# Performance work log

Measured on AMD Instinct MI355X. Metric: run time of the kernel, lower is better.

## Reference

```python
import jax, jax.numpy as jnp
import numpy as np

B, S, HID, NH, HD, INTER, NB = 4, 4096, 2048, 32, 64, 8192, 8
EPS = 1e-5
MEM_EPS = 1e-6


def rmsnorm(x, w, eps=EPS):
    return x * jax.lax.rsqrt(jnp.mean(x * x, axis=-1, keepdims=True) + eps) * w


def hbit_linear(x, w):
    # BitNet b1.58: ternary weights (absmean scale) + int8 per-token activation quant (STE).
    ws = jnp.mean(jnp.abs(w)) + 1e-8
    wq = jnp.round(jnp.clip(w / ws, -1.0, 1.0)) * ws
    w_eff = w + jax.lax.stop_gradient(wq - w)
    xs = 127.0 / jnp.clip(jnp.max(jnp.abs(x), axis=-1, keepdims=True), 1e-5, None)
    xq = jnp.clip(jnp.round(x * xs), -128.0, 127.0) / xs
    x_eff = x + jax.lax.stop_gradient(xq - x)
    return x_eff @ w_eff.T


def infini_attention(xn, wq, wk, wv, wo, beta):
    # xn: [B,S,HID]; segment-wise causal local attention + compressive linear memory.
    def proj(w):
        return (xn @ w.T).reshape(B, S, NH, HD).transpose(0, 2, 1, 3)  # [B,H,S,D]

    q, k, v = proj(wq), proj(wk), proj(wv)
    seg = S // NB

    def to_segs(t):
        return t.reshape(B, NH, NB, seg, HD).transpose(2, 0, 1, 3, 4)  # [NB,B,H,seg,D]

    qs, ks, vs = to_segs(q), to_segs(k), to_segs(v)
    mask = jnp.tril(jnp.ones((seg, seg), bool))
    g = jax.nn.sigmoid(beta)[None, :, None, None]  # per-head memory/local mix
    scale = 1.0 / np.sqrt(HD)

    def step(carry, inp):
        M, z = carry  # M:[B,H,D,D], z:[B,H,D]
        qc, kc, vc = inp
        sq = jax.nn.elu(qc) + 1.0
        sk = jax.nn.elu(kc) + 1.0
        a_mem = jnp.einsum('bhsd,bhde->bhse', sq, M) / (
            jnp.einsum('bhsd,bhd->bhs', sq, z)[..., None] + MEM_EPS)
        scores = jnp.einsum('bhqd,bhkd->bhqk', qc, kc) * scale
        scores = jnp.where(mask, scores, -1e9)
        a_loc = jnp.einsum('bhqk,bhkd->bhqd', jax.nn.softmax(scores, axis=-1), vc)
        M = M + jnp.einsum('bhsd,bhse->bhde', sk, vc)
        z = z + sk.sum(axis=2)
        out = g * a_mem + (1.0 - g) * a_loc
        return (M, z), out

    M0 = jnp.zeros((B, NH, HD, HD), xn.dtype)
    z0 = jnp.zeros((B, NH, HD), xn.dtype)
    _, outs = jax.lax.scan(step, (M0, z0), (qs, ks, vs))  # [NB,B,H,seg,D]
    out = outs.transpose(1, 2, 0, 3, 4).reshape(B, NH, S, HD)
    out = out.transpose(0, 2, 1, 3).reshape(B, S, HID)
    return out @ wo.T


def setup_inputs() -> dict:
    key = jax.random.key(0)
    ks = jax.random.split(key, 12)
    std = 0.02
    return {
        'x': jax.random.normal(ks[0], (B, S, HID), jnp.float32),
        'wq': jax.random.normal(ks[1], (HID, HID), jnp.float32) * std,
        'wk': jax.random.normal(ks[2], (HID, HID), jnp.float32) * std,
        'wv': jax.random.normal(ks[3], (HID, HID), jnp.float32) * std,
        'wo': jax.random.normal(ks[4], (HID, HID), jnp.float32) * std,
        'beta': jnp.zeros((NH,), jnp.float32),
        'gate': jnp.zeros((1,), jnp.float32),
        'attn_norm_w': jnp.ones((HID,), jnp.float32),
        'mlp_norm_w': jnp.ones((HID,), jnp.float32),
        'attn_res_norm_w': jnp.ones((HID,), jnp.float32),
        'attn_res_scale': jnp.full((1,), 0.1, jnp.float32),
        'mlp_res_norm_w': jnp.ones((HID,), jnp.float32),
        'mlp_res_scale': jnp.full((1,), 0.1, jnp.float32),
        'ffn_up_w': jax.random.normal(ks[5], (2 * INTER, HID), jnp.float32) * std,
        'ffn_down_w': jax.random.normal(ks[6], (HID, INTER), jnp.float32) * std,
    }


def reference(x, wq, wk, wv, wo, beta, gate, attn_norm_w, mlp_norm_w,
              attn_res_norm_w, attn_res_scale, mlp_res_norm_w, mlp_res_scale,
              ffn_up_w, ffn_down_w):
    residual = x
    xn = rmsnorm(x, attn_norm_w)
    infini_out = infini_attention(xn, wq, wk, wv, wo, beta)
    gated = jax.nn.sigmoid(gate) * infini_out
    x = residual + attn_res_scale * rmsnorm(gated, attn_res_norm_w)
    residual = x
    xn = rmsnorm(x, mlp_norm_w)
    up = hbit_linear(xn, ffn_up_w)
    gate_up, value = jnp.split(up, 2, axis=-1)
    mlp_out = hbit_linear(jax.nn.silu(gate_up) * value, ffn_down_w)
    x = residual + mlp_res_scale * rmsnorm(mlp_out, mlp_res_norm_w)
    return x
```

## Files before the change

### kernel.cpp

```cpp
#include <hip/hip_runtime.h>
#include <cstdint>
#include <cstddef>

typedef unsigned int u32;
typedef unsigned short u16;
typedef __bf16 bf16x8 __attribute__((ext_vector_type(8)));
typedef float f32x4 __attribute__((ext_vector_type(4)));
typedef float f32x16 __attribute__((ext_vector_type(16)));
typedef int i32x4 __attribute__((ext_vector_type(4)));

#define DEV static __device__ __forceinline__

DEV float bf2f(u16 u) { u32 x = ((u32)u) << 16; return __builtin_bit_cast(float, x); }
DEV u16 f2bf(float f) {
  u32 u = __builtin_bit_cast(u32, f);
  u32 r = (u + 0x7fffu + ((u >> 16) & 1u)) >> 16;
  return (u16)r;
}
DEV u32 pkbf(float a, float b) {
  __bf16 ba = (__bf16)a, bb = (__bf16)b;
  return (u32)__builtin_bit_cast(u16, ba) | ((u32)__builtin_bit_cast(u16, bb) << 16);
}
DEV u32 pk4i8(float a, float b, float c, float d) {
  return (u32)(unsigned char)(char)a | ((u32)(unsigned char)(char)b << 8) |
         ((u32)(unsigned char)(char)c << 16) | ((u32)(unsigned char)(char)d << 24);
}
DEV void bf8tof(const uint4 v, float* f) {
  f[0] = bf2f((u16)(v.x & 0xffffu)); f[1] = bf2f((u16)(v.x >> 16));
  f[2] = bf2f((u16)(v.y & 0xffffu)); f[3] = bf2f((u16)(v.y >> 16));
  f[4] = bf2f((u16)(v.z & 0xffffu)); f[5] = bf2f((u16)(v.z >> 16));
  f[6] = bf2f((u16)(v.w & 0xffffu)); f[7] = bf2f((u16)(v.w >> 16));
}
DEV uint4 f8tobf(const float* f) {
  uint4 r;
  r.x = (u32)f2bf(f[0]) | ((u32)f2bf(f[1]) << 16);
  r.y = (u32)f2bf(f[2]) | ((u32)f2bf(f[3]) << 16);
  r.z = (u32)f2bf(f[4]) | ((u32)f2bf(f[5]) << 16);
  r.w = (u32)f2bf(f[6]) | ((u32)f2bf(f[7]) << 16);
  return r;
}
DEV float sigmoidf_(float x) { return 1.f / (1.f + expf(-x)); }

DEV float wred_sum(float v) {
  #pragma unroll
  for (int m = 32; m; m >>= 1) v += __shfl_xor(v, m, 64);
  return v;
}
DEV float wred_max(float v) {
  #pragma unroll
  for (int m = 32; m; m >>= 1) v = fmaxf(v, __shfl_xor(v, m, 64));
  return v;
}
DEV float block_sum(float v, float* red, int nw) {
  v = wred_sum(v);
  int w = threadIdx.x >> 6, l = threadIdx.x & 63;
  if (l == 0) red[w] = v;
  __syncthreads();
  float t = red[0];
  for (int i = 1; i < nw; ++i) t += red[i];
  __syncthreads();
  return t;
}
DEV float block_max(float v, float* red, int nw) {
  v = wred_max(v);
  int w = threadIdx.x >> 6, l = threadIdx.x & 63;
  if (l == 0) red[w] = v;
  __syncthreads();
  float t = red[0];
  for (int i = 1; i < nw; ++i) t = fmaxf(t, red[i]);
  __syncthreads();
  return t;
}
DEV void gload16(const void* g, void* l) {
  __builtin_amdgcn_global_load_lds((const __attribute__((address_space(1))) void*)g,
                                   (__attribute__((address_space(3))) void*)l, 16, 0, 0);
}
DEV bf16x8 ldfrag(const u16* p) {
  uint4 u = *(const uint4*)p;
  return __builtin_bit_cast(bf16x8, u);
}

#define BN_ 4
#define S_ 4096
#define HID_ 2048
#define NH_ 32
#define HD_ 64
#define INTER_ 8192
#define NBSEG_ 8
#define SEG_ 512
#define TOK_ 16384
#define CHROWS_ 4096

__global__ __launch_bounds__(256) void castf2b(const float* __restrict__ a, u16* __restrict__ o) {
  size_t idx = ((size_t)blockIdx.x * 256 + threadIdx.x) * 4;
  float4 v = *(const float4*)(a + idx);
  float f[4] = {v.x, v.y, v.z, v.w};
  uint2 r;
  r.x = (u32)f2bf(f[0]) | ((u32)f2bf(f[1]) << 16);
  r.y = (u32)f2bf(f[2]) | ((u32)f2bf(f[3]) << 16);
  *(uint2*)(o + idx) = r;
}

__global__ __launch_bounds__(256) void absmean_part(const float* __restrict__ w, float* __restrict__ part) {
  __shared__ float red[4];
  size_t base = (size_t)blockIdx.x * 16384 + threadIdx.x * 4;
  float s = 0.f;
  #pragma unroll
  for (int i = 0; i < 16; ++i) {
    float4 v = *(const float4*)(w + base + (size_t)i * 1024);
    s += fabsf(v.x) + fabsf(v.y) + fabsf(v.z) + fabsf(v.w);
  }
  float t = block_sum(s, red, 4);
  if (threadIdx.x == 0) part[blockIdx.x] = t;
}

__global__ __launch_bounds__(256) void absmean_fin(const float* __restrict__ part, int n, float invN, float* __restrict__ outp) {
  __shared__ float red[4];
  float s = 0.f;
  for (int i = threadIdx.x; i < n; i += 256) s += part[i];
  float t = block_sum(s, red, 4);
  if (threadIdx.x == 0) outp[0] = t * invN + 1e-8f;
}

__global__ __launch_bounds__(256) void ternarize_i8(const float* __restrict__ w, const float* __restrict__ wsp, char* __restrict__ o) {
  size_t idx = ((size_t)blockIdx.x * 256 + threadIdx.x) * 4;
  const float inv = 1.f / wsp[0];
  float4 v = *(const float4*)(w + idx);
  float q0 = rintf(fminf(fmaxf(v.x * inv, -1.f), 1.f));
  float q1 = rintf(fminf(fmaxf(v.y * inv, -1.f), 1.f));
  float q2 = rintf(fminf(fmaxf(v.z * inv, -1.f), 1.f));
  float q3 = rintf(fminf(fmaxf(v.w * inv, -1.f), 1.f));
  *(u32*)(o + idx) = pk4i8(q0, q1, q2, q3);
}

__global__ __launch_bounds__(256) void rmsnorm_cast(const float* __restrict__ x, const float* __restrict__ wn, u16* __restrict__ o) {
  __shared__ float red[4];
  const int r = blockIdx.x, tid = threadIdx.x;
  const float* xr = x + (size_t)r * HID_;
  float vx[8];
  #pragma unroll
  for (int i = 0; i < 2; ++i) {
    float4 t = *(const float4*)(xr + tid * 8 + i * 4);
    vx[i * 4 + 0] = t.x; vx[i * 4 + 1] = t.y; vx[i * 4 + 2] = t.z; vx[i * 4 + 3] = t.w;
  }
  float ss = 0.f;
  #pragma unroll
  for (int j = 0; j < 8; ++j) ss += vx[j] * vx[j];
  float tot = block_sum(ss, red, 4);
  float rstd = rsqrtf(tot * (1.f / HID_) + 1e-5f);
  float wv[8];
  #pragma unroll
  for (int i = 0; i < 2; ++i) {
    float4 t = *(const float4*)(wn + tid * 8 + i * 4);
    wv[i * 4 + 0] = t.x; wv[i * 4 + 1] = t.y; wv[i * 4 + 2] = t.z; wv[i * 4 + 3] = t.w;
  }
  float ov[8];
  #pragma unroll
  for (int j = 0; j < 8; ++j) ov[j] = vx[j] * rstd * wv[j];
  *(uint4*)(o + (size_t)r * HID_ + tid * 8) = f8tobf(ov);
}

__global__ __launch_bounds__(256) void resid1_rms2(const float* __restrict__ x, const u16* __restrict__ ao,
    const float* __restrict__ gatep, const float* __restrict__ w1, const float* __restrict__ rsp,
    const float* __restrict__ w2, float* __restrict__ x2, char* __restrict__ xq, float* __restrict__ xs1) {
  __shared__ float red[4];
  const int r = blockIdx.x, tid = threadIdx.x;
  const float g = sigmoidf_(gatep[0]);
  const float rs = rsp[0];
  uint4 av = *(const uint4*)(ao + (size_t)r * HID_ + tid * 8);
  float f[8]; bf8tof(av, f);
  float ss = 0.f;
  #pragma unroll
  for (int j = 0; j < 8; ++j) { f[j] *= g; ss += f[j] * f[j]; }
  float tot = block_sum(ss, red, 4);
  float rstd1 = rsqrtf(tot * (1.f / HID_) + 1e-5f);
  const float* xr = x + (size_t)r * HID_;
  float xv2[8];
  #pragma unroll
  for (int i = 0; i < 2; ++i) {
    float4 xv = *(const float4*)(xr + tid * 8 + i * 4);
    float4 wv = *(const float4*)(w1 + tid * 8 + i * 4);
    xv2[i * 4 + 0] = xv.x + rs * f[i * 4 + 0] * rstd1 * wv.x;
    xv2[i * 4 + 1] = xv.y + rs * f[i * 4 + 1] * rstd1 * wv.y;
    xv2[i * 4 + 2] = xv.z + rs * f[i * 4 + 2] * rstd1 * wv.z;
    xv2[i * 4 + 3] = xv.w + rs * f[i * 4 + 3] * rstd1 * wv.w;
  }
  float* o = x2 + (size_t)r * HID_;
  *(float4*)(o + tid * 8) = float4{xv2[0], xv2[1], xv2[2], xv2[3]};
  *(float4*)(o + tid * 8 + 4) = float4{xv2[4], xv2[5], xv2[6], xv2[7]};
  float ss2 = 0.f;
  #pragma unroll
  for (int j = 0; j < 8; ++j) ss2 += xv2[j] * xv2[j];
  float tot2 = block_sum(ss2, red, 4);
  float rstd2 = rsqrtf(tot2 * (1.f / HID_) + 1e-5f);
  float xn[8]; float mx = 0.f;
  #pragma unroll
  for (int i = 0; i < 2; ++i) {
    float4 wv = *(const float4*)(w2 + tid * 8 + i * 4);
    xn[i * 4 + 0] = xv2[i * 4 + 0] * rstd2 * wv.x;
    xn[i * 4 + 1] = xv2[i * 4 + 1] * rstd2 * wv.y;
    xn[i * 4 + 2] = xv2[i * 4 + 2] * rstd2 * wv.z;
    xn[i * 4 + 3] = xv2[i * 4 + 3] * rstd2 * wv.w;
  }
  #pragma unroll
  for (int j = 0; j < 8; ++j) mx = fmaxf(mx, fabsf(xn[j]));
  float bm = block_max(mx, red, 4);
  float xs = 127.f / fmaxf(bm, 1e-5f);
  float q[8];
  #pragma unroll
  for (int j = 0; j < 8; ++j) q[j] = fminf(fmaxf(rintf(xn[j] * xs), -128.f), 127.f);
  uint2 pw;
  pw.x = pk4i8(q[0], q[1], q[2], q[3]);
  pw.y = pk4i8(q[4], q[5], q[6], q[7]);
  *(uint2*)(xq + (size_t)r * HID_ + tid * 8) = pw;
  if (tid == 0) xs1[r] = xs;
}

__global__ __launch_bounds__(256) void quant_h_i8(const u16* __restrict__ hb, char* __restrict__ hq, float* __restrict__ xs2) {
  __shared__ float red[4];
  const int r = blockIdx.x, tid = threadIdx.x;
  const u16* hr = hb + (size_t)r * INTER_ + tid * 32;
  float f[32];
  #pragma unroll
  for (int k = 0; k < 4; ++k) {
    uint4 v = *(const uint4*)(hr + k * 8);
    bf8tof(v, &f[k * 8]);
  }
  float mx = 0.f;
  #pragma unroll
  for (int j = 0; j < 32; ++j) mx = fmaxf(mx, fabsf(f[j]));
  float bm = block_max(mx, red, 4);
  float xs = 127.f / fmaxf(bm, 1e-5f);
  u32 pw[8];
  #pragma unroll
  for (int k = 0; k < 8; ++k) {
    float q[4];
    #pragma unroll
    for (int j = 0; j < 4; ++j) q[j] = fminf(fmaxf(rintf(f[k * 4 + j] * xs), -128.f), 127.f);
    pw[k] = pk4i8(q[0], q[1], q[2], q[3]);
  }
  char* oq = hq + (size_t)r * INTER_ + tid * 32;
  *(uint4*)oq = uint4{pw[0], pw[1], pw[2], pw[3]};
  *(uint4*)(oq + 16) = uint4{pw[4], pw[5], pw[6], pw[7]};
  if (tid == 0) xs2[r] = xs;
}

__global__ __launch_bounds__(256) void final_resid(const float* __restrict__ x2, const u16* __restrict__ mlp,
    const float* __restrict__ wn, const float* __restrict__ rsp, float* __restrict__ out) {
  __shared__ float red[4];
  const int r = blockIdx.x, tid = threadIdx.x;
  const float rs = rsp[0];
  uint4 mv = *(const uint4*)(mlp + (size_t)r * HID_ + tid * 8);
  float f[8]; bf8tof(mv, f);
  float ss = 0.f;
  #pragma unroll
  for (int j = 0; j < 8; ++j) ss += f[j] * f[j];
  float tot = block_sum(ss, red, 4);
  float rstd = rsqrtf(tot * (1.f / HID_) + 1e-5f);
  const float* xr = x2 + (size_t)r * HID_;
  float* o = out + (size_t)r * HID_;
  #pragma unroll
  for (int i = 0; i < 2; ++i) {
    float4 xv = *(const float4*)(xr + tid * 8 + i * 4);
    float4 wv = *(const float4*)(wn + tid * 8 + i * 4);
    float4 ov;
    ov.x = xv.x + rs * f[i * 4 + 0] * rstd * wv.x;
    ov.y = xv.y + rs * f[i * 4 + 1] * rstd * wv.y;
    ov.z = xv.z + rs * f[i * 4 + 2] * rstd * wv.z;
    ov.w = xv.w + rs * f[i * 4 + 3] * rstd * wv.w;
    *(float4*)(o + tid * 8 + i * 4) = ov;
  }
}

template<int MODE>
__global__ __launch_bounds__(256)
void gemm_bt(const u16* __restrict__ A, const u16* __restrict__ Bw, u16* __restrict__ C,
             int N, int K, const float* __restrict__ wsp, const float* __restrict__ xs) {
  __shared__ __align__(16) u16 As[128 * 32];
  __shared__ __align__(16) u16 Bs[128 * 32];
  const int tid = threadIdx.x;
  const int wv = tid >> 6, lane = tid & 63;
  const int l15 = lane & 15, l4 = lane >> 4;
  const int wr = (wv >> 1) * 64, wc = (wv & 1) * 64;
  const int bm = blockIdx.x, bn = blockIdx.y;
  const u16* Ag = A + (size_t)bm * 128 * K;
  const u16* Bg = Bw + (size_t)bn * 128 * K;
  const int c0 = tid, c1 = tid + 256;
  f32x4 acc[4][4] = {};
  for (int kk = 0; kk < K; kk += 32) {
    gload16(Ag + (size_t)(c0 >> 2) * K + kk + (c0 & 3) * 8, &As[c0 * 8]);
    gload16(Ag + (size_t)(c1 >> 2) * K + kk + (c1 & 3) * 8, &As[c1 * 8]);
    gload16(Bg + (size_t)(c0 >> 2) * K + kk + (c0 & 3) * 8, &Bs[c0 * 8]);
    gload16(Bg + (size_t)(c1 >> 2) * K + kk + (c1 & 3) * 8, &Bs[c1 * 8]);
    __syncthreads();
    bf16x8 af[4], bb[4];
    #pragma unroll
    for (int i = 0; i < 4; ++i) af[i] = ldfrag(&As[(wr + i * 16 + l15) * 32 + l4 * 8]);
    #pragma unroll
    for (int j = 0; j < 4; ++j) bb[j] = ldfrag(&Bs[(wc + j * 16 + l15) * 32 + l4 * 8]);
    #pragma unroll
    for (int i = 0; i < 4; ++i)
      #pragma unroll
      for (int j = 0; j < 4; ++j)
        acc[i][j] = __builtin_amdgcn_mfma_f32_16x16x32_bf16(af[i], bb[j], acc[i][j], 0, 0, 0);
    __syncthreads();
  }
  #pragma unroll
  for (int i = 0; i < 4; ++i) {
    #pragma unroll
    for (int r = 0; r < 4; ++r) {
      const int row = bm * 128 + wr + i * 16 + l4 * 4 + r;
      #pragma unroll
      for (int j = 0; j < 4; ++j) {
        const int col = bn * 128 + wc + j * 16 + l15;
        C[(size_t)row * N + col] = f2bf(acc[i][j][r]);
      }
    }
  }
}

__global__ __launch_bounds__(512, 2)
void gemm_up_i8(const char* __restrict__ A, const char* __restrict__ Bw, u16* __restrict__ H,
                const float* __restrict__ wsp, const float* __restrict__ xs) {
  const int K = HID_;
  __shared__ __align__(16) char As[128 * 128];
  __shared__ __align__(16) char Gs[128 * 128];
  __shared__ __align__(16) char Vs[128 * 128];
  const int tid = threadIdx.x;
  const int w = tid >> 6, lane = tid & 63;
  const int l15 = lane & 15, l4 = lane >> 4;
  const int wr = (w >> 2) * 64, wc = (w & 3) * 32;
  int id = blockIdx.x;
  const int cpx = (int)gridDim.x >> 3;
  id = (id & 7) * cpx + (id >> 3);
  const int bm = id & 31, bn = id >> 5;
  const char* Ag = A + (size_t)bm * 128 * K;
  const char* Gg = Bw + (size_t)bn * 128 * K;
  const char* Vg = Bw + ((size_t)INTER_ + bn * 128) * K;
  i32x4 ag[4][2] = {}, av[4][2] = {};
  for (int kk = 0; kk < K; kk += 128) {
    #pragma unroll
    for (int p = 0; p < 2; ++p) {
      const int idx = tid + p * 512;
      const int row = idx >> 3, slot = idx & 7;
      const int ss = slot ^ (row & 7);
      gload16(Ag + (size_t)row * K + kk + ss * 16, &As[idx * 16]);
      gload16(Gg + (size_t)row * K + kk + ss * 16, &Gs[idx * 16]);
      gload16(Vg + (size_t)row * K + kk + ss * 16, &Vs[idx * 16]);
    }
    __syncthreads();
    i32x4 af_[4][2], gf_[2][2], vf_[2][2];
    #pragma unroll
    for (int i = 0; i < 4; ++i) {
      const int r = wr + i * 16 + l15;
      #pragma unroll
      for (int k2 = 0; k2 < 2; ++k2) {
        const int j = k2 * 4 + l4;
        af_[i][k2] = *(const i32x4*)&As[r * 128 + ((j ^ (r & 7)) * 16)];
      }
    }
    #pragma unroll
    for (int jj = 0; jj < 2; ++jj) {
      const int r = wc + jj * 16 + l15;
      #pragma unroll
      for (int k2 = 0; k2 < 2; ++k2) {
        const int j = k2 * 4 + l4;
        gf_[jj][k2] = *(const i32x4*)&Gs[r * 128 + ((j ^ (r & 7)) * 16)];
        vf_[jj][k2] = *(const i32x4*)&Vs[r * 128 + ((j ^ (r & 7)) * 16)];
      }
    }
    #pragma unroll
    for (int i = 0; i < 4; ++i)
      #pragma unroll
      for (int jj = 0; jj < 2; ++jj)
        #pragma unroll
        for (int k2 = 0; k2 < 2; ++k2) {
          ag[i][jj] = __builtin_amdgcn_mfma_i32_16x16x64_i8(af_[i][k2], gf_[jj][k2], ag[i][jj], 0, 0, 0);
          av[i][jj] = __builtin_amdgcn_mfma_i32_16x16x64_i8(af_[i][k2], vf_[jj][k2], av[i][jj], 0, 0, 0);
        }
    __syncthreads();
  }
  const float ws0 = wsp[0];
  #pragma unroll
  for (int i = 0; i < 4; ++i) {
    #pragma unroll
    for (int r = 0; r < 4; ++r) {
      const int row = bm * 128 + wr + i * 16 + l4 * 4 + r;
      const float scl = ws0 / xs[row];
      #pragma unroll
      for (int jj = 0; jj < 2; ++jj) {
        const int col = bn * 128 + wc + jj * 16 + l15;
        const float og = (float)ag[i][jj][r] * scl;
        const float ov = (float)av[i][jj][r] * scl;
        const float hv = og * ov / (1.f + expf(-og));
        H[(size_t)row * INTER_ + col] = f2bf(hv);
      }
    }
  }
}

__global__ __launch_bounds__(256, 2)
void gemm_dn_i8(const char* __restrict__ A, const char* __restrict__ Bw, u16* __restrict__ C,
                const float* __restrict__ wsp, const float* __restrict__ xs) {
  const int N = HID_, K = INTER_;
  __shared__ __align__(16) char As[128 * 128];
  __shared__ __align__(16) char Bs[128 * 128];
  const int tid = threadIdx.x;
  const int wv = tid >> 6, lane = tid & 63;
  const int l15 = lane & 15, l4 = lane >> 4;
  const int wr = (wv >> 1) * 64, wc = (wv & 1) * 64;
  const int bm = blockIdx.x, bn = blockIdx.y;
  const char* Ag = A + (size_t)bm * 128 * K;
  const char* Bg = Bw + (size_t)bn * 128 * K;
  i32x4 acc[4][4] = {};
  for (int kk = 0; kk < K; kk += 128) {
    #pragma unroll
    for (int p = 0; p < 4; ++p) {
      const int idx = tid + p * 256;
      const int row = idx >> 3, slot = idx & 7;
      const int ss = slot ^ (row & 7);
      gload16(Ag + (size_t)row * K + kk + ss * 16, &As[idx * 16]);
      gload16(Bg + (size_t)row * K + kk + ss * 16, &Bs[idx * 16]);
    }
    __syncthreads();
    i32x4 af_[4][2], bb_[4][2];
    #pragma unroll
    for (int i = 0; i < 4; ++i) {
      const int ra = wr + i * 16 + l15;
      const int rb = wc + i * 16 + l15;
      #pragma unroll
      for (int k2 = 0; k2 < 2; ++k2) {
        const int j = k2 * 4 + l4;
        af_[i][k2] = *(const i32x4*)&As[ra * 128 + ((j ^ (ra & 7)) * 16)];
        bb_[i][k2] = *(const i32x4*)&Bs[rb * 128 + ((j ^ (rb & 7)) * 16)];
      }
    }
    #pragma unroll
    for (int i = 0; i < 4; ++i)
      #pragma unroll
      for (int j = 0; j < 4; ++j)
        #pragma unroll
        for (int k2 = 0; k2 < 2; ++k2)
          acc[i][j] = __builtin_amdgcn_mfma_i32_16x16x64_i8(af_[i][k2], bb_[j][k2], acc[i][j], 0, 0, 0);
    __syncthreads();
  }
  const float ws0 = wsp[0];
  #pragma unroll
  for (int i = 0; i < 4; ++i) {
    #pragma unroll
    for (int r = 0; r < 4; ++r) {
      const int row = bm * 128 + wr + i * 16 + l4 * 4 + r;
      const float scl = ws0 / xs[row];
      #pragma unroll
      for (int j = 0; j < 4; ++j) {
        const int col = bn * 128 + wc + j * 16 + l15;
        C[(size_t)row * N + col] = f2bf((float)acc[i][j][r] * scl);
      }
    }
  }
}

DEV void write_otile(const f32x16 oc, float invl, char* stgB, u16* alocrow,
                     int da, int l31, int hi, int lane) {
  #pragma unroll
  for (int r = 0; r < 16; ++r) {
    const int dl = (r & 3) + 8 * (r >> 2) + 4 * hi;
    *(u16*)(stgB + l31 * 64 + ((dl * 2) ^ ((l31 & 3) << 4))) = f2bf(oc[r] * invl);
  }
  #pragma unroll
  for (int p = 0; p < 2; ++p) {
    const int s = lane >> 1;
    const int d8 = (lane & 1) * 8 + p * 16;
    const uint4 val = *(const uint4*)(stgB + s * 64 + ((d8 * 2) ^ ((s & 3) << 4)));
    *(uint4*)(alocrow + (size_t)s * HD_ + da * 32 + d8) = val;
  }
}

__global__ __launch_bounds__(512)
void attn_local_mfma(const u16* __restrict__ q, const u16* __restrict__ k, const u16* __restrict__ v,
                     u16* __restrict__ aloc, float* __restrict__ Useg, float* __restrict__ yseg) {
  __shared__ __align__(16) u16 Ks[512 * 64];
  __shared__ __align__(16) u16 VT[64 * 512];
  __shared__ __align__(16) u16 SP[9216];
  const int bid = blockIdx.x;
  const int c = bid >> 7, bh = bid & 127;
  const int b = bh >> 5, h = bh & 31;
  const int tid = threadIdx.x, w = tid >> 6, lane = tid & 63;
  const int l31 = lane & 31, hi = lane >> 5;
  const size_t rowbase = ((size_t)b * S_ + c * SEG_) * (size_t)HID_ + h * HD_;
  const u16* qg = q + rowbase;
  const u16* kg = k + rowbase;
  const u16* vg = v + rowbase;
  char* KsB = (char*)Ks;
  char* VTB = (char*)VT;
  #pragma unroll
  for (int p = 0; p < 8; ++p) {
    const int idx = tid + p * 512;
    const int t = idx >> 3, dg = idx & 7;
    const uint4 kv = *(const uint4*)(kg + (size_t)t * HID_ + dg * 8);
    *(uint4*)(KsB + t * 128 + ((dg * 16) ^ ((t & 7) << 4))) = kv;
  }
  {
    const int t = w * 64 + lane;
    #pragma unroll
    for (int dg = 0; dg < 8; ++dg) {
      const uint4 vv = *(const uint4*)(vg + (size_t)t * HID_ + dg * 8);
      const u16* e = (const u16*)&vv;
      #pragma unroll
      for (int j = 0; j < 8; ++j) {
        const int d = dg * 8 + j;
        *(u16*)(VTB + d * 1024 + ((t * 2) ^ ((d & 7) << 4))) = e[j];
      }
    }
  }
  uint4 qf[2][4];
  #pragma unroll
  for (int qi = 0; qi < 2; ++qi)
    #pragma unroll
    for (int ks = 0; ks < 4; ++ks)
      qf[qi][ks] = *(const uint4*)(qg + (size_t)(w * 64 + qi * 32 + l31) * HID_ + ks * 16 + hi * 8);
  __syncthreads();

  const size_t arow = (size_t)(b * NH_ + h) * S_ + c * SEG_;
  const int swzk = (l31 & 7) << 4;
  char* stgB = (char*)SP + w * 2048;
  #pragma unroll
  for (int qi = 0; qi < 2; ++qi) {
    f32x16 o0 = {}, o1 = {};
    float m = -3e38f, l = 0.f;
    const int nb = w * 2 + qi + 1;
    for (int tb = 0; tb < nb; ++tb) {
      f32x16 st = {};
      #pragma unroll
      for (int ks = 0; ks < 4; ++ks) {
        const uint4 ka = *(const uint4*)(KsB + (tb * 32 + l31) * 128 + (((ks * 16 + hi * 8) * 2) ^ swzk));
        st = __builtin_amdgcn_mfma_f32_32x32x16_bf16(__builtin_bit_cast(bf16x8, ka),
                                                     __builtin_bit_cast(bf16x8, qf[qi][ks]), st, 0, 0, 0);
      }
      if (tb == nb - 1) {
        #pragma unroll
        for (int r = 0; r < 16; ++r) {
          const int tl = (r & 3) + 8 * (r >> 2) + 4 * hi;
          if (tl > l31) st[r] = -3e38f;
        }
      }
      float tm = st[0];
      #pragma unroll
      for (int r = 1; r < 16; ++r) tm = fmaxf(tm, st[r]);
      tm = fmaxf(tm, __shfl_xor(tm, 32, 64));
      const float mn = fmaxf(m, tm);
      const float fac = __expf((m - mn) * 0.125f);
      float pr[16]; float ps = 0.f;
      #pragma unroll
      for (int r = 0; r < 16; ++r) { pr[r] = __expf((st[r] - mn) * 0.125f); ps += pr[r]; }
      ps += __shfl_xor(ps, 32, 64);
      l = l * fac + ps;
      m = mn;
      #pragma unroll
      for (int r = 0; r < 16; ++r) { o0[r] *= fac; o1[r] *= fac; }
      #pragma unroll
      for (int c2 = 0; c2 < 2; ++c2) {
        const int bi = c2 * 8;
        const u32 a0 = pkbf(pr[bi + 0], pr[bi + 1]);
        const u32 a1 = pkbf(pr[bi + 2], pr[bi + 3]);
        const u32 a2 = pkbf(pr[bi + 4], pr[bi + 5]);
        const u32 a3 = pkbf(pr[bi + 6], pr[bi + 7]);
        const u32 x0 = (u32)__shfl_xor((int)a0, 32, 64);
        const u32 x1 = (u32)__shfl_xor((int)a1, 32, 64);
        const u32 x2 = (u32)__shfl_xor((int)a2, 32, 64);
        const u32 x3 = (u32)__shfl_xor((int)a3, 32, 64);
        uint4 pw;
        pw.x = hi ? x2 : a0;
        pw.y = hi ? x3 : a1;
        pw.z = hi ? a2 : x0;
        pw.w = hi ? a3 : x1;
        const bf16x8 pfr = __builtin_bit_cast(bf16x8, pw);
        const int tO = (tb * 32 + c2 * 16 + hi * 8) * 2;
        const uint4 v0 = *(const uint4*)(VTB + l31 * 1024 + (tO ^ swzk));
        const uint4 v1 = *(const uint4*)(VTB + (32 + l31) * 1024 + (tO ^ swzk));
        o0 = __builtin_amdgcn_mfma_f32_32x32x16_bf16(__builtin_bit_cast(bf16x8, v0), pfr, o0, 0, 0, 0);
        o1 = __builtin_amdgcn_mfma_f32_32x32x16_bf16(__builtin_bit_cast(bf16x8, v1), pfr, o1, 0, 0, 0);
      }
    }
    const float invl = 1.f / l;
    u16* alocrow = aloc + (arow + w * 64 + qi * 32) * HD_;
    write_otile(o0, invl, stgB, alocrow, 0, l31, hi, lane);
    write_otile(o1, invl, stgB, alocrow, 1, l31, hi, lane);
  }

  __syncthreads();
  float* Ured = (float*)SP;
  float* yred = (float*)((char*)SP + 16384);
  for (int i = tid; i < 4096; i += 512) Ured[i] = 0.f;
  yred[tid] = 0.f;
  __syncthreads();
  f32x16 u00 = {}, u01 = {}, u10 = {}, u11 = {};
  float y0 = 0.f, y1 = 0.f;
  #pragma unroll
  for (int kc = 0; kc < 4; ++kc) {
    const int t0 = w * 64 + kc * 16 + hi * 8;
    uint4 af[2];
    #pragma unroll
    for (int da2 = 0; da2 < 2; ++da2) {
      const int d = da2 * 32 + l31;
      u32 wds[4];
      #pragma unroll
      for (int jp = 0; jp < 4; ++jp) {
        const int ta = t0 + jp * 2;
        const int tb2 = ta + 1;
        const float kfa = bf2f(*(const u16*)(KsB + ta * 128 + ((d * 2) ^ ((ta & 7) << 4))));
        const float kfb = bf2f(*(const u16*)(KsB + tb2 * 128 + ((d * 2) ^ ((tb2 & 7) << 4))));
        const float sa = kfa > 0.f ? kfa + 1.f : __expf(kfa);
        const float sb = kfb > 0.f ? kfb + 1.f : __expf(kfb);
        if (da2 == 0) y0 += sa + sb; else y1 += sa + sb;
        wds[jp] = pkbf(sa, sb);
      }
      af[da2].x = wds[0]; af[da2].y = wds[1]; af[da2].z = wds[2]; af[da2].w = wds[3];
    }
    const int tO = t0 * 2;
    const uint4 vb0 = *(const uint4*)(VTB + l31 * 1024 + (tO ^ swzk));
    const uint4 vb1 = *(const uint4*)(VTB + (32 + l31) * 1024 + (tO ^ swzk));
    const bf16x8 a0f = __builtin_bit_cast(bf16x8, af[0]);
    const bf16x8 a1f = __builtin_bit_cast(bf16x8, af[1]);
    const bf16x8 b0f = __builtin_bit_cast(bf16x8, vb0);
    const bf16x8 b1f = __builtin_bit_cast(bf16x8, vb1);
    u00 = __builtin_amdgcn_mfma_f32_32x32x16_bf16(a0f, b0f, u00, 0, 0, 0);
    u01 = __builtin_amdgcn_mfma_f32_32x32x16_bf16(a0f, b1f, u01, 0, 0, 0);
    u10 = __builtin_amdgcn_mfma_f32_32x32x16_bf16(a1f, b0f, u10, 0, 0, 0);
    u11 = __builtin_amdgcn_mfma_f32_32x32x16_bf16(a1f, b1f, u11, 0, 0, 0);
  }
  y0 += __shfl_xor(y0, 32, 64);
  y1 += __shfl_xor(y1, 32, 64);
  if (hi == 0) { yred[w * 64 + l31] = y0; yred[w * 64 + 32 + l31] = y1; }
  for (int ww = 0; ww < 8; ++ww) {
    if (w == ww) {
      #pragma unroll
      for (int r = 0; r < 16; ++r) {
        const int dl = (r & 3) + 8 * (r >> 2) + 4 * hi;
        Ured[dl * 64 + l31]            += u00[r];
        Ured[dl * 64 + 32 + l31]       += u01[r];
        Ured[(32 + dl) * 64 + l31]     += u10[r];
        Ured[(32 + dl) * 64 + 32 + l31]+= u11[r];
      }
    }
    __syncthreads();
  }
  float* Ug = Useg + (size_t)(c * 128 + bh) * 4096;
  for (int i = tid; i < 4096; i += 512) Ug[i] = Ured[i];
  if (tid < 64) {
    float a2 = 0.f;
    #pragma unroll
    for (int ww = 0; ww < 8; ++ww) a2 += yred[ww * 64 + tid];
    yseg[(size_t)(c * 128 + bh) * 64 + tid] = a2;
  }
}

__global__ __launch_bounds__(256)
void attn_prefix(const float* __restrict__ Useg, const float* __restrict__ yseg,
                 float* __restrict__ Mpre, float* __restrict__ zpre) {
  const int bh = blockIdx.x, tid = threadIdx.x;
  for (int idx = tid; idx < 4096; idx += 256) {
    float a2 = 0.f;
    #pragma unroll
    for (int c = 0; c < 8; ++c) {
      const size_t o = ((size_t)(c * 128 + bh)) * 4096 + idx;
      Mpre[o] = a2;
      a2 += Useg[o];
    }
  }
  if (tid < 64) {
    float a2 = 0.f;
    #pragma unroll
    for (int c = 0; c < 8; ++c) {
      const size_t o = ((size_t)(c * 128 + bh)) * 64 + tid;
      zpre[o] = a2;
      a2 += yseg[o];
    }
  }
}

__global__ __launch_bounds__(512)
void attn_combine(const u16* __restrict__ q, const u16* __restrict__ aloc,
                  const float* __restrict__ Mpre, const float* __restrict__ zpre,
                  const float* __restrict__ beta, u16* __restrict__ attno) {
  __shared__ __align__(16) u16 MbT[64 * 64];
  __shared__ float z_lds[64];
  __shared__ float amem[8][16 * 65];
  const int bid = blockIdx.x;
  const int c = bid >> 7, bh = bid & 127;
  const int b = bh >> 5, h = bh & 31;
  const int tid = threadIdx.x, w = tid >> 6, lane = tid & 63;
  const int l15 = lane & 15, l4 = lane >> 4;
  const size_t pre = (size_t)(c * 128 + bh);
  char* MbB = (char*)MbT;
  for (int i = tid; i < 4096; i += 512) {
    const int d = i >> 6, e = i & 63;
    *(u16*)(MbB + (((e * 64 + d) * 2) ^ ((e & 7) << 4))) = f2bf(Mpre[pre * 4096 + i]);
  }
  if (tid < 64) z_lds[tid] = zpre[pre * 64 + tid];
  __syncthreads();
  bf16x8 bb[2][4];
  #pragma unroll
  for (int ks = 0; ks < 2; ++ks)
    #pragma unroll
    for (int jt = 0; jt < 4; ++jt) {
      const int e = jt * 16 + l15;
      const uint4 u = *(const uint4*)(MbB + (((e * 64 + ks * 32 + l4 * 8) * 2) ^ ((e & 7) << 4)));
      bb[ks][jt] = __builtin_bit_cast(bf16x8, u);
    }
  const float g = sigmoidf_(beta[h]);
  const float og = 1.f - g;
  const u16* qg = q + ((size_t)b * S_ + c * SEG_) * HID_ + h * HD_;
  const size_t arow = (size_t)(b * NH_ + h) * S_ + c * SEG_;
  u16* orow = attno + ((size_t)b * S_ + c * SEG_) * HID_ + h * HD_;
  const int rr = lane >> 2, cq = (lane & 3) * 16;
  #pragma unroll
  for (int mi = 0; mi < 4; ++mi) {
    const int s0 = w * 64 + mi * 16;
    f32x4 acc[4] = {};
    float pd = 0.f;
    #pragma unroll
    for (int ks = 0; ks < 2; ++ks) {
      const uint4 qv = *(const uint4*)(qg + (size_t)(s0 + l15) * HID_ + ks * 32 + l4 * 8);
      float f[8]; bf8tof(qv, f);
      float sq[8];
      #pragma unroll
      for (int j = 0; j < 8; ++j) {
        sq[j] = f[j] > 0.f ? f[j] + 1.f : __expf(f[j]);
        pd = fmaf(sq[j], z_lds[ks * 32 + l4 * 8 + j], pd);
      }
      uint4 pw;
      pw.x = pkbf(sq[0], sq[1]); pw.y = pkbf(sq[2], sq[3]);
      pw.z = pkbf(sq[4], sq[5]); pw.w = pkbf(sq[6], sq[7]);
      const bf16x8 af = __builtin_bit_cast(bf16x8, pw);
      #pragma unroll
      for (int jt = 0; jt < 4; ++jt)
        acc[jt] = __builtin_amdgcn_mfma_f32_16x16x32_bf16(af, bb[ks][jt], acc[jt], 0, 0, 0);
    }
    pd += __shfl_xor(pd, 16, 64);
    pd += __shfl_xor(pd, 32, 64);
    pd += 1e-6f;
    float dinv[4];
    #pragma unroll
    for (int r = 0; r < 4; ++r) dinv[r] = 1.f / __shfl(pd, l4 * 4 + r, 64);
    #pragma unroll
    for (int jt = 0; jt < 4; ++jt)
      #pragma unroll
      for (int r = 0; r < 4; ++r)
        amem[w][(l4 * 4 + r) * 65 + jt * 16 + l15] = acc[jt][r] * dinv[r];
    const int s = s0 + rr;
    const u16* alr = aloc + (arow + s) * HD_ + cq;
    const uint4 a0 = *(const uint4*)alr;
    const uint4 a1 = *(const uint4*)(alr + 8);
    float alf[16];
    bf8tof(a0, alf); bf8tof(a1, alf + 8);
    float ov[16];
    #pragma unroll
    for (int t = 0; t < 16; ++t)
      ov[t] = g * amem[w][rr * 65 + cq + t] + og * alf[t];
    *(uint4*)(orow + (size_t)s * HID_ + cq) = f8tobf(ov);
    *(uint4*)(orow + (size_t)s * HID_ + cq + 8) = f8tobf(ov + 8);
  }
}

extern "C" void kernel_launch(void* const* d_in, const int* in_sizes, int n_in,
                              void* d_out, int out_size, void* d_ws, size_t ws_size,
                              hipStream_t stream) {
  const float* x    = (const float*)d_in[0];
  const float* wq   = (const float*)d_in[1];
  const float* wk   = (const float*)d_in[2];
  const float* wv   = (const float*)d_in[3];
  const float* wo   = (const float*)d_in[4];
  const float* beta = (const float*)d_in[5];
  const float* gate = (const float*)d_in[6];
  const float* anw  = (const float*)d_in[7];
  const float* mnw  = (const float*)d_in[8];
  const float* arnw = (const float*)d_in[9];
  const float* arsc = (const float*)d_in[10];
  const float* mrnw = (const float*)d_in[11];
  const float* mrsc = (const float*)d_in[12];
  const float* fup  = (const float*)d_in[13];
  const float* fdn  = (const float*)d_in[14];

  char* W = (char*)d_ws;
  const size_t MB = 1ull << 20;
  u16*   xn1   = (u16*)(W + 0);
  u16*   attno = (u16*)(W + 0);
  u16*   mlpb  = (u16*)(W + 0);
  u16*   qb    = (u16*)(W + 64 * MB);
  char*  xq1   = (char*)(W + 64 * MB);
  u16*   kb    = (u16*)(W + 128 * MB);
  u16*   aob   = (u16*)(W + 128 * MB);
  u16*   hbuf  = (u16*)(W + 128 * MB);
  u16*   vb    = (u16*)(W + 192 * MB);
  u16*   alocb = (u16*)(W + 256 * MB);
  float* x2    = (float*)(W + 192 * MB);
  float* Useg  = (float*)(W + 320 * MB);
  float* Mpre  = (float*)(W + 336 * MB);
  float* yseg  = (float*)(W + 352 * MB);
  float* zpre  = (float*)(W + 352 * MB + 262144);
  float* xs1   = (float*)(W + 352 * MB + 524288);
  float* xs2   = (float*)(W + 352 * MB + 589824);
  float* wsu   = (float*)(W + 352 * MB + 655360);
  float* wsd   = (float*)(W + 352 * MB + 655616);
  float* partU = (float*)(W + 352 * MB + 655872);
  float* partD = (float*)(W + 352 * MB + 664064);
  u16*   w16q  = (u16*)(W + 353 * MB);
  u16*   w16k  = (u16*)(W + 361 * MB);
  u16*   w16v  = (u16*)(W + 369 * MB);
  u16*   w16o  = (u16*)(W + 377 * MB);
  char*  wqup  = (char*)(W + 385 * MB);
  char*  wqdn  = (char*)(W + 417 * MB);
  char*  hq    = (char*)(W + 433 * MB);

  castf2b<<<4096, 256, 0, stream>>>(wq, w16q);
  castf2b<<<4096, 256, 0, stream>>>(wk, w16k);
  castf2b<<<4096, 256, 0, stream>>>(wv, w16v);
  castf2b<<<4096, 256, 0, stream>>>(wo, w16o);
  absmean_part<<<2048, 256, 0, stream>>>(fup, partU);
  absmean_part<<<1024, 256, 0, stream>>>(fdn, partD);
  absmean_fin<<<1, 256, 0, stream>>>(partU, 2048, 1.f / 33554432.f, wsu);
  absmean_fin<<<1, 256, 0, stream>>>(partD, 1024, 1.f / 16777216.f, wsd);
  ternarize_i8<<<32768, 256, 0, stream>>>(fup, wsu, wqup);
  ternarize_i8<<<16384, 256, 0, stream>>>(fdn, wsd, wqdn);

  rmsnorm_cast<<<16384, 256, 0, stream>>>(x, anw, xn1);
  gemm_bt<0><<<dim3(128, 16), 256, 0, stream>>>(xn1, w16q, qb, HID_, HID_, nullptr, nullptr);
  gemm_bt<0><<<dim3(128, 16), 256, 0, stream>>>(xn1, w16k, kb, HID_, HID_, nullptr, nullptr);
  gemm_bt<0><<<dim3(128, 16), 256, 0, stream>>>(xn1, w16v, vb, HID_, HID_, nullptr, nullptr);
  attn_local_mfma<<<1024, 512, 0, stream>>>(qb, kb, vb, alocb, Useg, yseg);
  attn_prefix<<<128, 256, 0, stream>>>(Useg, yseg, Mpre, zpre);
  attn_combine<<<1024, 512, 0, stream>>>(qb, alocb, Mpre, zpre, beta, attno);
  gemm_bt<0><<<dim3(128, 16), 256, 0, stream>>>(attno, w16o, aob, HID_, HID_, nullptr, nullptr);
  resid1_rms2<<<16384, 256, 0, stream>>>(x, aob, gate, arnw, arsc, mnw, x2, xq1, xs1);

  for (int cc = 0; cc < 4; ++cc) {
    const size_t base = (size_t)cc * CHROWS_;
    gemm_up_i8<<<2048, 512, 0, stream>>>(xq1 + base * HID_, wqup, hbuf, wsu, xs1 + base);
    quant_h_i8<<<4096, 256, 0, stream>>>(hbuf, hq, xs2 + base);
    gemm_dn_i8<<<dim3(32, 16), 256, 0, stream>>>(hq, wqdn, mlpb + base * HID_, wsd, xs2 + base);
  }
  final_resid<<<16384, 256, 0, stream>>>(x2, mlpb, mrnw, mrsc, (float*)d_out);
}
```

Before: 2.268 ms.

## Fuse QKV projections into one GEMM and widen K-tile with swizzled LDS

```diff
diff --git a/kernel.cpp b/kernel.cpp
--- a/kernel.cpp
+++ b/kernel.cpp
@@ -90,6 +90,7 @@
 #define SEG_ 512
 #define TOK_ 16384
 #define CHROWS_ 4096
+#define LDQ_ 6144
 
 __global__ __launch_bounds__(256) void castf2b(const float* __restrict__ a, u16* __restrict__ o) {
   size_t idx = ((size_t)blockIdx.x * 256 + threadIdx.x) * 4;
@@ -272,12 +273,11 @@
   }
 }
 
-template<int MODE>
 __global__ __launch_bounds__(256)
 void gemm_bt(const u16* __restrict__ A, const u16* __restrict__ Bw, u16* __restrict__ C,
-             int N, int K, const float* __restrict__ wsp, const float* __restrict__ xs) {
-  __shared__ __align__(16) u16 As[128 * 32];
-  __shared__ __align__(16) u16 Bs[128 * 32];
+             int K, int ldc) {
+  __shared__ __align__(16) u16 As[128 * 64];
+  __shared__ __align__(16) u16 Bs[128 * 64];
   const int tid = threadIdx.x;
   const int wv = tid >> 6, lane = tid & 63;
   const int l15 = lane & 15, l4 = lane >> 4;
@@ -285,24 +285,36 @@
   const int bm = blockIdx.x, bn = blockIdx.y;
   const u16* Ag = A + (size_t)bm * 128 * K;
   const u16* Bg = Bw + (size_t)bn * 128 * K;
-  const int c0 = tid, c1 = tid + 256;
   f32x4 acc[4][4] = {};
-  for (int kk = 0; kk < K; kk += 32) {
-    gload16(Ag + (size_t)(c0 >> 2) * K + kk + (c0 & 3) * 8, &As[c0 * 8]);
-    gload16(Ag + (size_t)(c1 >> 2) * K + kk + (c1 & 3) * 8, &As[c1 * 8]);
-    gload16(Bg + (size_t)(c0 >> 2) * K + kk + (c0 & 3) * 8, &Bs[c0 * 8]);
-    gload16(Bg + (size_t)(c1 >> 2) * K + kk + (c1 & 3) * 8, &Bs[c1 * 8]);
+  for (int kk = 0; kk < K; kk += 64) {
+    #pragma unroll
+    for (int p = 0; p < 4; ++p) {
+      const int idx = tid + p * 256;
+      const int row = idx >> 3, slot = idx & 7;
+      const int ss = slot ^ (row & 7);
+      gload16(Ag + (size_t)row * K + kk + ss * 8, &As[idx * 8]);
+      gload16(Bg + (size_t)row * K + kk + ss * 8, &Bs[idx * 8]);
+    }
     __syncthreads();
-    bf16x8 af[4], bb[4];
-    #pragma unroll
-    for (int i = 0; i < 4; ++i) af[i] = ldfrag(&As[(wr + i * 16 + l15) * 32 + l4 * 8]);
-    #pragma unroll
-    for (int j = 0; j < 4; ++j) bb[j] = ldfrag(&Bs[(wc + j * 16 + l15) * 32 + l4 * 8]);
+    bf16x8 af[4][2], bb[4][2];
+    #pragma unroll
+    for (int i = 0; i < 4; ++i) {
+      const int ra = wr + i * 16 + l15;
+      const int rb = wc + i * 16 + l15;
+      #pragma unroll
+      for (int k2 = 0; k2 < 2; ++k2) {
+        const int g8 = k2 * 4 + l4;
+        af[i][k2] = ldfrag(&As[ra * 64 + ((g8 ^ (ra & 7)) * 8)]);
+        bb[i][k2] = ldfrag(&Bs[rb * 64 + ((g8 ^ (rb & 7)) * 8)]);
+      }
+    }
     #pragma unroll
     for (int i = 0; i < 4; ++i)
       #pragma unroll
       for (int j = 0; j < 4; ++j)
-        acc[i][j] = __builtin_amdgcn_mfma_f32_16x16x32_bf16(af[i], bb[j], acc[i][j], 0, 0, 0);
+        #pragma unroll
+        for (int k2 = 0; k2 < 2; ++k2)
+          acc[i][j] = __builtin_amdgcn_mfma_f32_16x16x32_bf16(af[i][k2], bb[j][k2], acc[i][j], 0, 0, 0);
     __syncthreads();
   }
   #pragma unroll
@@ -313,7 +325,7 @@
       #pragma unroll
       for (int j = 0; j < 4; ++j) {
         const int col = bn * 128 + wc + j * 16 + l15;
-        C[(size_t)row * N + col] = f2bf(acc[i][j][r]);
+        C[(size_t)row * ldc + col] = f2bf(acc[i][j][r]);
       }
     }
   }
@@ -478,7 +490,7 @@
 
 __global__ __launch_bounds__(512)
 void attn_local_mfma(const u16* __restrict__ q, const u16* __restrict__ k, const u16* __restrict__ v,
-                     u16* __restrict__ aloc, float* __restrict__ Useg, float* __restrict__ yseg) {
+                     u16* __restrict__ aloc, float* __restrict__ Useg, float* __restrict__ yseg, int ldq) {
   __shared__ __align__(16) u16 Ks[512 * 64];
   __shared__ __align__(16) u16 VT[64 * 512];
   __shared__ __align__(16) u16 SP[9216];
@@ -487,7 +499,7 @@
   const int b = bh >> 5, h = bh & 31;
   const int tid = threadIdx.x, w = tid >> 6, lane = tid & 63;
   const int l31 = lane & 31, hi = lane >> 5;
-  const size_t rowbase = ((size_t)b * S_ + c * SEG_) * (size_t)HID_ + h * HD_;
+  const size_t rowbase = ((size_t)b * S_ + c * SEG_) * (size_t)ldq + h * HD_;
   const u16* qg = q + rowbase;
   const u16* kg = k + rowbase;
   const u16* vg = v + rowbase;
@@ -497,14 +509,14 @@
   for (int p = 0; p < 8; ++p) {
     const int idx = tid + p * 512;
     const int t = idx >> 3, dg = idx & 7;
-    const uint4 kv = *(const uint4*)(kg + (size_t)t * HID_ + dg * 8);
+    const uint4 kv = *(const uint4*)(kg + (size_t)t * ldq + dg * 8);
     *(uint4*)(KsB + t * 128 + ((dg * 16) ^ ((t & 7) << 4))) = kv;
   }
   {
     const int t = w * 64 + lane;
     #pragma unroll
     for (int dg = 0; dg < 8; ++dg) {
-      const uint4 vv = *(const uint4*)(vg + (size_t)t * HID_ + dg * 8);
+      const uint4 vv = *(const uint4*)(vg + (size_t)t * ldq + dg * 8);
       const u16* e = (const u16*)&vv;
       #pragma unroll
       for (int j = 0; j < 8; ++j) {
@@ -518,7 +530,7 @@
   for (int qi = 0; qi < 2; ++qi)
     #pragma unroll
     for (int ks = 0; ks < 4; ++ks)
-      qf[qi][ks] = *(const uint4*)(qg + (size_t)(w * 64 + qi * 32 + l31) * HID_ + ks * 16 + hi * 8);
+      qf[qi][ks] = *(const uint4*)(qg + (size_t)(w * 64 + qi * 32 + l31) * ldq + ks * 16 + hi * 8);
   __syncthreads();
 
   const size_t arow = (size_t)(b * NH_ + h) * S_ + c * SEG_;
@@ -682,7 +694,7 @@
 __global__ __launch_bounds__(512)
 void attn_combine(const u16* __restrict__ q, const u16* __restrict__ aloc,
                   const float* __restrict__ Mpre, const float* __restrict__ zpre,
-                  const float* __restrict__ beta, u16* __restrict__ attno) {
+                  const float* __restrict__ beta, u16* __restrict__ attno, int ldq) {
   __shared__ __align__(16) u16 MbT[64 * 64];
   __shared__ float z_lds[64];
   __shared__ float amem[8][16 * 65];
@@ -710,7 +722,7 @@
     }
   const float g = sigmoidf_(beta[h]);
   const float og = 1.f - g;
-  const u16* qg = q + ((size_t)b * S_ + c * SEG_) * HID_ + h * HD_;
+  const u16* qg = q + ((size_t)b * S_ + c * SEG_) * ldq + h * HD_;
   const size_t arow = (size_t)(b * NH_ + h) * S_ + c * SEG_;
   u16* orow = attno + ((size_t)b * S_ + c * SEG_) * HID_ + h * HD_;
   const int rr = lane >> 2, cq = (lane & 3) * 16;
@@ -721,7 +733,7 @@
     float pd = 0.f;
     #pragma unroll
     for (int ks = 0; ks < 2; ++ks) {
-      const uint4 qv = *(const uint4*)(qg + (size_t)(s0 + l15) * HID_ + ks * 32 + l4 * 8);
+      const uint4 qv = *(const uint4*)(qg + (size_t)(s0 + l15) * ldq + ks * 32 + l4 * 8);
       float f[8]; bf8tof(qv, f);
       float sq[8];
       #pragma unroll
@@ -787,12 +799,10 @@
   u16*   xn1   = (u16*)(W + 0);
   u16*   attno = (u16*)(W + 0);
   u16*   mlpb  = (u16*)(W + 0);
-  u16*   qb    = (u16*)(W + 64 * MB);
+  u16*   qkv   = (u16*)(W + 64 * MB);
   char*  xq1   = (char*)(W + 64 * MB);
-  u16*   kb    = (u16*)(W + 128 * MB);
   u16*   aob   = (u16*)(W + 128 * MB);
   u16*   hbuf  = (u16*)(W + 128 * MB);
-  u16*   vb    = (u16*)(W + 192 * MB);
   u16*   alocb = (u16*)(W + 256 * MB);
   float* x2    = (float*)(W + 192 * MB);
   float* Useg  = (float*)(W + 320 * MB);
@@ -805,17 +815,15 @@
   float* wsd   = (float*)(W + 352 * MB + 655616);
   float* partU = (float*)(W + 352 * MB + 655872);
   float* partD = (float*)(W + 352 * MB + 664064);
-  u16*   w16q  = (u16*)(W + 353 * MB);
-  u16*   w16k  = (u16*)(W + 361 * MB);
-  u16*   w16v  = (u16*)(W + 369 * MB);
+  u16*   w16qkv= (u16*)(W + 353 * MB);
   u16*   w16o  = (u16*)(W + 377 * MB);
   char*  wqup  = (char*)(W + 385 * MB);
   char*  wqdn  = (char*)(W + 417 * MB);
   char*  hq    = (char*)(W + 433 * MB);
 
-  castf2b<<<4096, 256, 0, stream>>>(wq, w16q);
-  castf2b<<<4096, 256, 0, stream>>>(wk, w16k);
-  castf2b<<<4096, 256, 0, stream>>>(wv, w16v);
+  castf2b<<<4096, 256, 0, stream>>>(wq, w16qkv);
+  castf2b<<<4096, 256, 0, stream>>>(wk, w16qkv + (size_t)HID_ * HID_);
+  castf2b<<<4096, 256, 0, stream>>>(wv, w16qkv + 2 * (size_t)HID_ * HID_);
   castf2b<<<4096, 256, 0, stream>>>(wo, w16o);
   absmean_part<<<2048, 256, 0, stream>>>(fup, partU);
   absmean_part<<<1024, 256, 0, stream>>>(fdn, partD);
@@ -825,13 +833,11 @@
   ternarize_i8<<<16384, 256, 0, stream>>>(fdn, wsd, wqdn);
 
   rmsnorm_cast<<<16384, 256, 0, stream>>>(x, anw, xn1);
-  gemm_bt<0><<<dim3(128, 16), 256, 0, stream>>>(xn1, w16q, qb, HID_, HID_, nullptr, nullptr);
-  gemm_bt<0><<<dim3(128, 16), 256, 0, stream>>>(xn1, w16k, kb, HID_, HID_, nullptr, nullptr);
-  gemm_bt<0><<<dim3(128, 16), 256, 0, stream>>>(xn1, w16v, vb, HID_, HID_, nullptr, nullptr);
-  attn_local_mfma<<<1024, 512, 0, stream>>>(qb, kb, vb, alocb, Useg, yseg);
+  gemm_bt<<<dim3(128, 48), 256, 0, stream>>>(xn1, w16qkv, qkv, HID_, LDQ_);
+  attn_local_mfma<<<1024, 512, 0, stream>>>(qkv, qkv + HID_, qkv + 2 * HID_, alocb, Useg, yseg, LDQ_);
   attn_prefix<<<128, 256, 0, stream>>>(Useg, yseg, Mpre, zpre);
-  attn_combine<<<1024, 512, 0, stream>>>(qb, alocb, Mpre, zpre, beta, attno);
-  gemm_bt<0><<<dim3(128, 16), 256, 0, stream>>>(attno, w16o, aob, HID_, HID_, nullptr, nullptr);
+  attn_combine<<<1024, 512, 0, stream>>>(qkv, alocb, Mpre, zpre, beta, attno, LDQ_);
+  gemm_bt<<<dim3(128, 16), 256, 0, stream>>>(attno, w16o, aob, HID_, HID_);
   resid1_rms2<<<16384, 256, 0, stream>>>(x, aob, gate, arnw, arsc, mnw, x2, xq1, xs1);
 
   for (int cc = 0; cc < 4; ++cc) {
```

Result: faster. 2.094 ms (-7.6%).
